# Performance work log

Hardware: AMD Instinct MI355X
Metric: run time of the kernel (lower is better)

Reference implementation:

```python
import jax, jax.numpy as jnp
import numpy as np

B, T, D_MODEL, N_HEADS = 2, 2048, 1024, 16
HEAD_DIM = D_MODEL // N_HEADS
EPS = 1e-6
ROPE_BASE = 10000.0


def _rope_cos_sin(seq_len, dim, offset=0, dtype=jnp.float32):
    half = dim // 2
    inv_freq = 1.0 / (ROPE_BASE ** (jnp.arange(half, dtype=jnp.float32) / half))
    pos = jnp.arange(offset, offset + seq_len, dtype=jnp.float32)
    freqs = pos[:, None] * inv_freq[None, :]              # (T, half)
    emb = jnp.concatenate([freqs, freqs], axis=-1)        # (T, dim)
    return jnp.cos(emb).astype(dtype), jnp.sin(emb).astype(dtype)


def _rotate_half(x):
    x1, x2 = jnp.split(x, 2, axis=-1)
    return jnp.concatenate([-x2, x1], axis=-1)


def setup_inputs() -> dict:
    key = jax.random.key(0)
    k1, k2, k3 = jax.random.split(key, 3)
    x = jax.random.normal(k1, (B, T, D_MODEL), dtype=jnp.float32)
    norm_w = jnp.ones((D_MODEL,), dtype=jnp.float32)
    w_qkv = jax.random.normal(k2, (3 * D_MODEL, D_MODEL), dtype=jnp.float32) * 0.02
    w_out = jax.random.normal(k3, (D_MODEL, D_MODEL), dtype=jnp.float32) * 0.02
    return {"x": x, "norm_w": norm_w, "w_qkv": w_qkv, "w_out": w_out}


def reference(x, norm_w, w_qkv, w_out):
    # RMSNorm (pre-norm)
    h = x * jax.lax.rsqrt(jnp.mean(jnp.square(x), axis=-1, keepdims=True) + EPS) * norm_w
    # Fused QKV projection: (B,T,3*D)
    qkv = jnp.einsum('btd,ed->bte', h, w_qkv).reshape(B, T, 3, N_HEADS, HEAD_DIM)
    q, k, v = qkv[:, :, 0], qkv[:, :, 1], qkv[:, :, 2]   # each (B,T,H,Dh)
    # RoPE on q, k (offset=0)
    cos, sin = _rope_cos_sin(T, HEAD_DIM, dtype=q.dtype)
    cos = cos[None, :, None, :]
    sin = sin[None, :, None, :]
    q = q * cos + _rotate_half(q) * sin
    k = k * cos + _rotate_half(k) * sin
    # Causal scaled dot-product attention
    scale = 1.0 / np.sqrt(HEAD_DIM)
    scores = jnp.einsum('bqhd,bkhd->bhqk', q, k) * scale  # (B,H,T,T)
    causal = jnp.tril(jnp.ones((T, T), dtype=bool))
    scores = jnp.where(causal[None, None], scores, jnp.finfo(scores.dtype).min)
    attn = jax.nn.softmax(scores, axis=-1)
    out = jnp.einsum('bhqk,bkhd->bqhd', attn, v).reshape(B, T, D_MODEL)
    out = jnp.einsum('btd,ed->bte', out, w_out)
    return x + out
```

## Files before the change

### kernel.cpp

```cpp
#include <hip/hip_runtime.h>
#include <math.h>

typedef unsigned short u16;
typedef unsigned int u32;
typedef __attribute__((ext_vector_type(4))) float f32x4;
typedef __attribute__((ext_vector_type(8))) short s16x8;

#define GLL16(g, l) __builtin_amdgcn_global_load_lds( \
    (const __attribute__((address_space(1))) void*)(g), \
    (__attribute__((address_space(3))) void*)(l), 16, 0, 0)

__device__ __forceinline__ u16 f2bf(float f) {
  union { float f; u32 u; } v; v.f = f;
  u32 r = v.u + 0x7FFFu + ((v.u >> 16) & 1u);
  return (u16)(r >> 16);
}
__device__ __forceinline__ float bf2f(u16 h) {
  union { u32 u; float f; } v; v.u = ((u32)h) << 16;
  return v.f;
}
__device__ __forceinline__ u32 pk2bf(float lo, float hi) {
  union { float f; u32 u; } a, b; a.f = lo; b.f = hi;
  return __builtin_amdgcn_perm(b.u + 0x8000u, a.u + 0x8000u, 0x07060302u);
}
__device__ __forceinline__ float fexp2(float x) {
#if __has_builtin(__builtin_amdgcn_exp2f)
  return __builtin_amdgcn_exp2f(x);
#else
  return exp2f(x);
#endif
}

__global__ __launch_bounds__(256) void cast_kernel(const float* __restrict__ src,
                                                   u16* __restrict__ dst, int n4) {
  int i = blockIdx.x * 256 + threadIdx.x;
  if (i >= n4) return;
  float4 v = ((const float4*)src)[i];
  uint2 o;
  o.x = (u32)f2bf(v.x) | ((u32)f2bf(v.y) << 16);
  o.y = (u32)f2bf(v.z) | ((u32)f2bf(v.w) << 16);
  ((uint2*)dst)[i] = o;
}

__global__ __launch_bounds__(256) void rmsnorm_kernel(const float* __restrict__ x,
                                                      const float* __restrict__ wgt,
                                                      u16* __restrict__ h) {
  const int row = blockIdx.x, tid = threadIdx.x;
  const float4 v = *(const float4*)&x[(size_t)row * 1024 + tid * 4];
  float ss = v.x * v.x + v.y * v.y + v.z * v.z + v.w * v.w;
  ss += __shfl_xor(ss, 1);  ss += __shfl_xor(ss, 2);  ss += __shfl_xor(ss, 4);
  ss += __shfl_xor(ss, 8);  ss += __shfl_xor(ss, 16); ss += __shfl_xor(ss, 32);
  __shared__ float red[4];
  if ((tid & 63) == 0) red[tid >> 6] = ss;
  __syncthreads();
  const float tot = red[0] + red[1] + red[2] + red[3];
  const float s = rsqrtf(tot * (1.0f / 1024.0f) + 1e-6f);
  const float4 g = *(const float4*)&wgt[tid * 4];
  uint2 o;
  o.x = (u32)f2bf(v.x * s * g.x) | ((u32)f2bf(v.y * s * g.y) << 16);
  o.y = (u32)f2bf(v.z * s * g.z) | ((u32)f2bf(v.w * s * g.w) << 16);
  *(uint2*)&h[(size_t)row * 1024 + tid * 4] = o;
}

template <int EPI>
__global__ __launch_bounds__(256) void gemm_bt(const u16* __restrict__ A,
                                               const u16* __restrict__ Bt,
                                               u16* __restrict__ Cb,
                                               float* __restrict__ Cf,
                                               const float* __restrict__ resid,
                                               int M, int N, int K) {
  __shared__ __attribute__((aligned(16))) u16 As[128 * 32];
  __shared__ __attribute__((aligned(16))) u16 Bs[128 * 32];
  const int tid = threadIdx.x;
  const int w = tid >> 6, lane = tid & 63;
  const int quad = lane >> 4, l16 = lane & 15;
  const int gm0 = blockIdx.y * 128, gn0 = blockIdx.x * 128;
  const int wm = (w & 1) * 64, wn = (w >> 1) * 64;

  f32x4 acc[4][4] = {};

  for (int k0 = 0; k0 < K; k0 += 32) {
    __syncthreads();
    if (w < 2) {
      #pragma unroll
      for (int i = 0; i < 4; ++i) {
        int sb = (w * 4 + i) * 64;
        int slot = sb + lane;
        int m = slot >> 2, c = (slot & 3) ^ (m & 3);
        GLL16(A + (size_t)(gm0 + m) * K + k0 + c * 8, &As[sb * 8]);
      }
    } else {
      #pragma unroll
      for (int i = 0; i < 4; ++i) {
        int sb = ((w - 2) * 4 + i) * 64;
        int slot = sb + lane;
        int n = slot >> 2, c = (slot & 3) ^ (n & 3);
        GLL16(Bt + (size_t)(gn0 + n) * K + k0 + c * 8, &Bs[sb * 8]);
      }
    }
    __syncthreads();
    s16x8 aF[4], bF[4];
    #pragma unroll
    for (int i = 0; i < 4; ++i) {
      int m = wm + i * 16 + l16;
      aF[i] = *(const s16x8*)&As[(m * 4 + (quad ^ (m & 3))) * 8];
    }
    #pragma unroll
    for (int j = 0; j < 4; ++j) {
      int n = wn + j * 16 + l16;
      bF[j] = *(const s16x8*)&Bs[(n * 4 + (quad ^ (n & 3))) * 8];
    }
    #pragma unroll
    for (int i = 0; i < 4; ++i)
      #pragma unroll
      for (int j = 0; j < 4; ++j)
        acc[i][j] = __builtin_amdgcn_mfma_f32_16x16x32_bf16(aF[i], bF[j], acc[i][j], 0, 0, 0);
  }

  #pragma unroll
  for (int i = 0; i < 4; ++i) {
    int row0 = gm0 + wm + i * 16 + quad * 4;
    #pragma unroll
    for (int j = 0; j < 4; ++j) {
      int col = gn0 + wn + j * 16 + l16;
      #pragma unroll
      for (int r = 0; r < 4; ++r) {
        size_t idx = (size_t)(row0 + r) * N + col;
        if (EPI == 0) Cb[idx] = f2bf(acc[i][j][r]);
        else          Cf[idx] = acc[i][j][r] + resid[idx];
      }
    }
  }
}

__global__ __launch_bounds__(256) void rope_kernel(const u16* __restrict__ qkv,
                                                   u16* __restrict__ Qr,
                                                   u16* __restrict__ Kr,
                                                   u16* __restrict__ Vt) {
  const int tt = blockIdx.x, bh = blockIdx.y;
  const int b = bh >> 4, h = bh & 15;
  const int tid = threadIdx.x;
  const float QSCALE = 0.125f * 1.4426950408889634f;

  #pragma unroll
  for (int ii = 0; ii < 8; ++ii) {
    int idx = ii * 256 + tid;
    int tl = idx >> 5, jj = idx & 31;
    int t = tt * 64 + tl;
    size_t mrow = (size_t)(b * 2048 + t) * 3072 + h * 64;
    float q1 = bf2f(qkv[mrow + jj]),        q2 = bf2f(qkv[mrow + 32 + jj]);
    float k1 = bf2f(qkv[mrow + 1024 + jj]), k2 = bf2f(qkv[mrow + 1024 + 32 + jj]);
    float invf = exp2f(-(float)jj * (13.287712379549449f / 32.0f));
    float ang = (float)t * invf;
    float sn, cs;
    sincosf(ang, &sn, &cs);
    size_t orow = (size_t)(bh * 2048 + t) * 64;
    Qr[orow + jj]      = f2bf((q1 * cs - q2 * sn) * QSCALE);
    Qr[orow + 32 + jj] = f2bf((q2 * cs + q1 * sn) * QSCALE);
    Kr[orow + jj]      = f2bf(k1 * cs - k2 * sn);
    Kr[orow + 32 + jj] = f2bf(k2 * cs + k1 * sn);
  }

  __shared__ __attribute__((aligned(16))) u16 Vl[64][72];
  for (int s = tid; s < 512; s += 256) {
    int r = s >> 3, c8 = (s & 7) * 8;
    *(uint4*)&Vl[r][c8] =
        *(const uint4*)&qkv[(size_t)(b * 2048 + tt * 64 + r) * 3072 + 2048 + h * 64 + c8];
  }
  __syncthreads();
  for (int s = tid; s < 512; s += 256) {
    int d = s >> 3, t8 = (s & 7) * 8;
    u16 tmp[8];
    #pragma unroll
    for (int k = 0; k < 8; ++k) tmp[k] = Vl[t8 + k][d];
    *(uint4*)&Vt[(size_t)(bh * 64 + d) * 2048 + tt * 64 + t8] = *(uint4*)tmp;
  }
}

__global__ __launch_bounds__(256) void attn_kernel(const u16* __restrict__ Qr,
                                                   const u16* __restrict__ Kr,
                                                   const u16* __restrict__ Vt,
                                                   u16* __restrict__ AO) {
  __shared__ __attribute__((aligned(16))) char smem[51200];
  const int tid = threadIdx.x;
  const int w = tid >> 6, lane = tid & 63;
  const int quad = lane >> 4, l16 = lane & 15;
  const int id = blockIdx.x;
  const int bh = id & 31;
  const int qhv = id >> 5;
  const int qblk = (qhv < 8) ? (15 - 2 * qhv) : (2 * qhv - 16);
  const int b = bh >> 4, h = bh & 15;
  const size_t qkb = (size_t)bh * (2048 * 64);
  const size_t vtb = (size_t)bh * (64 * 2048);
  const int q0 = qblk * 128;
  const int q0w = q0 + w * 32;
  const int jmax = 2 * qblk + 1;
  u16* Pw = (u16*)(smem + 32768 + w * 4608);

  s16x8 bQ[2][2];
  #pragma unroll
  for (int s = 0; s < 2; ++s)
    #pragma unroll
    for (int hf = 0; hf < 2; ++hf)
      bQ[s][hf] = *(const s16x8*)&Qr[qkb + (size_t)(q0w + s * 16 + l16) * 64 + hf * 32 + quad * 8];

  f32x4 O[2][4] = {};
  float l_run[2] = {0.0f, 0.0f};

  const int srow = lane >> 3;
  const int scg = (lane & 7) ^ srow;

  auto STAGE = [&](int jn, int nxt) {
    if (w < 2) {
      #pragma unroll
      for (int ii = 0; ii < 4; ++ii) {
        int i = w * 4 + ii;
        GLL16(Kr + qkb + (size_t)(jn * 64 + i * 8 + srow) * 64 + scg * 8,
              smem + nxt * 8192 + i * 1024);
      }
    } else {
      #pragma unroll
      for (int ii = 0; ii < 4; ++ii) {
        int i = (w - 2) * 4 + ii;
        GLL16(Vt + vtb + (size_t)(i * 8 + srow) * 2048 + jn * 64 + scg * 8,
              smem + 16384 + nxt * 8192 + i * 1024);
      }
    }
  };

  STAGE(0, 0);
  __syncthreads();
  int cur = 0;

  for (int j = 0; j <= jmax; ++j) {
    if (j < jmax) STAGE(j + 1, cur ^ 1);

    if (j * 64 <= q0w + 31) {
      const u16* Kb = (const u16*)(smem + cur * 8192);
      const u16* Vb = (const u16*)(smem + 16384 + cur * 8192);
      const bool masked = (j * 64 + 63 > q0w);
      const int rsw = (l16 & 7);

      s16x8 aK[4][2];
      #pragma unroll
      for (int kt = 0; kt < 4; ++kt)
        #pragma unroll
        for (int hf = 0; hf < 2; ++hf)
          aK[kt][hf] = *(const s16x8*)&Kb[(kt * 16 + l16) * 64 + (((hf * 4 + quad) ^ rsw) * 8)];

      f32x4 S[2][4];
      __builtin_amdgcn_s_setprio(1);
      #pragma unroll
      for (int kt = 0; kt < 4; ++kt)
        #pragma unroll
        for (int s = 0; s < 2; ++s) {
          f32x4 z = {};
          z = __builtin_amdgcn_mfma_f32_16x16x32_bf16(aK[kt][0], bQ[s][0], z, 0, 0, 0);
          S[s][kt] = __builtin_amdgcn_mfma_f32_16x16x32_bf16(aK[kt][1], bQ[s][1], z, 0, 0, 0);
        }
      __builtin_amdgcn_s_setprio(0);

      if (masked) {
        #pragma unroll
        for (int s = 0; s < 2; ++s) {
          int q = q0w + s * 16 + l16;
          #pragma unroll
          for (int kt = 0; kt < 4; ++kt) {
            int key0 = j * 64 + kt * 16 + quad * 4;
            #pragma unroll
            for (int r = 0; r < 4; ++r)
              if (key0 + r > q) S[s][kt][r] = -1e30f;
          }
        }
      }

      #pragma unroll
      for (int s = 0; s < 2; ++s) {
        float sum = 0.0f;
        #pragma unroll
        for (int kt = 0; kt < 4; ++kt) {
          #pragma unroll
          for (int r = 0; r < 4; ++r) {
            float e = fexp2(S[s][kt][r]);
            S[s][kt][r] = e;
            sum += e;
          }
        }
        sum += __shfl_xor(sum, 16);
        sum += __shfl_xor(sum, 32);
        l_run[s] += sum;
        #pragma unroll
        for (int kt = 0; kt < 4; ++kt) {
          uint2 pw;
          pw.x = pk2bf(S[s][kt][0], S[s][kt][1]);
          pw.y = pk2bf(S[s][kt][2], S[s][kt][3]);
          *(uint2*)&Pw[s * 1152 + l16 * 72 + kt * 16 + quad * 4] = pw;
        }
      }

      s16x8 bP[2][2];
      #pragma unroll
      for (int s = 0; s < 2; ++s) {
        bP[s][0] = *(const s16x8*)&Pw[s * 1152 + l16 * 72 + quad * 8];
        bP[s][1] = *(const s16x8*)&Pw[s * 1152 + l16 * 72 + 32 + quad * 8];
      }
      s16x8 aV[4][2];
      #pragma unroll
      for (int dt = 0; dt < 4; ++dt)
        #pragma unroll
        for (int hf = 0; hf < 2; ++hf)
          aV[dt][hf] = *(const s16x8*)&Vb[(dt * 16 + l16) * 64 + (((hf * 4 + quad) ^ rsw) * 8)];

      __builtin_amdgcn_s_setprio(1);
      #pragma unroll
      for (int dt = 0; dt < 4; ++dt)
        #pragma unroll
        for (int s = 0; s < 2; ++s) {
          O[s][dt] = __builtin_amdgcn_mfma_f32_16x16x32_bf16(aV[dt][0], bP[s][0], O[s][dt], 0, 0, 0);
          O[s][dt] = __builtin_amdgcn_mfma_f32_16x16x32_bf16(aV[dt][1], bP[s][1], O[s][dt], 0, 0, 0);
        }
      __builtin_amdgcn_s_setprio(0);
    }

    __syncthreads();
    cur ^= 1;
  }

  #pragma unroll
  for (int s = 0; s < 2; ++s) {
    float inv = __builtin_amdgcn_rcpf(l_run[s]);
    int q = q0w + s * 16 + l16;
    #pragma unroll
    for (int dt = 0; dt < 4; ++dt) {
      uint2 ow;
      ow.x = pk2bf(O[s][dt][0] * inv, O[s][dt][1] * inv);
      ow.y = pk2bf(O[s][dt][2] * inv, O[s][dt][3] * inv);
      *(uint2*)&AO[(size_t)(b * 2048 + q) * 1024 + h * 64 + dt * 16 + quad * 4] = ow;
    }
  }
}

extern "C" void kernel_launch(void* const* d_in, const int* in_sizes, int n_in,
                              void* d_out, int out_size, void* d_ws, size_t ws_size,
                              hipStream_t stream) {
  const float* x      = (const float*)d_in[0];
  const float* norm_w = (const float*)d_in[1];
  const float* w_qkv  = (const float*)d_in[2];
  const float* w_out  = (const float*)d_in[3];
  float* out = (float*)d_out;

  u16* ws     = (u16*)d_ws;
  u16* wqkv_b = ws;
  u16* wout_b = wqkv_b + 3145728;
  u16* h_b    = wout_b + 1048576;
  u16* qkv_b  = h_b + 4194304;
  u16* Qr     = qkv_b + 12582912;
  u16* Kr     = Qr + 4194304;
  u16* Vt     = Kr + 4194304;
  u16* AO     = Vt + 4194304;

  cast_kernel<<<3072, 256, 0, stream>>>(w_qkv, wqkv_b, 786432);
  cast_kernel<<<1024, 256, 0, stream>>>(w_out, wout_b, 262144);
  rmsnorm_kernel<<<4096, 256, 0, stream>>>(x, norm_w, h_b);
  gemm_bt<0><<<dim3(24, 32), 256, 0, stream>>>(h_b, wqkv_b, qkv_b, nullptr, nullptr,
                                               4096, 3072, 1024);
  rope_kernel<<<dim3(32, 32), 256, 0, stream>>>(qkv_b, Qr, Kr, Vt);
  attn_kernel<<<512, 256, 0, stream>>>(Qr, Kr, Vt, AO);
  gemm_bt<1><<<dim3(8, 32), 256, 0, stream>>>(AO, wout_b, nullptr, out, x,
                                              4096, 1024, 1024);
}
```

Before: 196.5 us.

## Split attention KV range across two wave groups and pair causal query blocks

The attention kernel now uses 512 threads per block: two groups of four waves each process alternating 64-key tiles for the same 128-query block and merge their partial O and row sums through shared memory at the end. Each block also handles a pair of complementary query blocks (c and 15-c) in sequence, which balances the causal work, and the grid shrinks to 256 blocks. The aim is more parallelism per query block and better load balance. The cost is double the LDS footprint (100KB), an extra reduction pass, and lower block count, which may hurt occupancy.

Result: faster. 190.8 us (-2.9%).

```diff
diff --git a/kernel.cpp b/kernel.cpp
--- a/kernel.cpp
+++ b/kernel.cpp
@@ -177,166 +177,190 @@
   }
 }
 
-__global__ __launch_bounds__(256) void attn_kernel(const u16* __restrict__ Qr,
+__global__ __launch_bounds__(512) void attn_kernel(const u16* __restrict__ Qr,
                                                    const u16* __restrict__ Kr,
                                                    const u16* __restrict__ Vt,
                                                    u16* __restrict__ AO) {
-  __shared__ __attribute__((aligned(16))) char smem[51200];
+  __shared__ __attribute__((aligned(16))) char smem[102400];
   const int tid = threadIdx.x;
   const int w = tid >> 6, lane = tid & 63;
+  const int wq = w & 3, wp = w >> 2;
   const int quad = lane >> 4, l16 = lane & 15;
   const int id = blockIdx.x;
   const int bh = id & 31;
-  const int qhv = id >> 5;
-  const int qblk = (qhv < 8) ? (15 - 2 * qhv) : (2 * qhv - 16);
+  const int c  = id >> 5;
   const int b = bh >> 4, h = bh & 15;
   const size_t qkb = (size_t)bh * (2048 * 64);
   const size_t vtb = (size_t)bh * (64 * 2048);
-  const int q0 = qblk * 128;
-  const int q0w = q0 + w * 32;
-  const int jmax = 2 * qblk + 1;
-  u16* Pw = (u16*)(smem + 32768 + w * 4608);
-
-  s16x8 bQ[2][2];
-  #pragma unroll
-  for (int s = 0; s < 2; ++s)
-    #pragma unroll
-    for (int hf = 0; hf < 2; ++hf)
-      bQ[s][hf] = *(const s16x8*)&Qr[qkb + (size_t)(q0w + s * 16 + l16) * 64 + hf * 32 + quad * 8];
-
-  f32x4 O[2][4] = {};
-  float l_run[2] = {0.0f, 0.0f};
+  u16* Pw = (u16*)(smem + 65536 + w * 4608);
 
   const int srow = lane >> 3;
-  const int scg = (lane & 7) ^ srow;
-
-  auto STAGE = [&](int jn, int nxt) {
-    if (w < 2) {
+  const int scg  = (lane & 7) ^ srow;
+  const int smat = w & 1, stp = (w >> 1) & 1, shalf = (w >> 2) & 1;
+
+  auto STAGE = [&](int j0, int d) {
+    const int jn = j0 + stp;
+    if (smat == 0) {
       #pragma unroll
       for (int ii = 0; ii < 4; ++ii) {
-        int i = w * 4 + ii;
+        int i = shalf * 4 + ii;
         GLL16(Kr + qkb + (size_t)(jn * 64 + i * 8 + srow) * 64 + scg * 8,
-              smem + nxt * 8192 + i * 1024);
+              smem + (stp * 2 + d) * 8192 + i * 1024);
       }
     } else {
       #pragma unroll
       for (int ii = 0; ii < 4; ++ii) {
-        int i = (w - 2) * 4 + ii;
+        int i = shalf * 4 + ii;
         GLL16(Vt + vtb + (size_t)(i * 8 + srow) * 2048 + jn * 64 + scg * 8,
-              smem + 16384 + nxt * 8192 + i * 1024);
+              smem + 32768 + (stp * 2 + d) * 8192 + i * 1024);
       }
     }
   };
 
-  STAGE(0, 0);
-  __syncthreads();
-  int cur = 0;
-
-  for (int j = 0; j <= jmax; ++j) {
-    if (j < jmax) STAGE(j + 1, cur ^ 1);
-
-    if (j * 64 <= q0w + 31) {
-      const u16* Kb = (const u16*)(smem + cur * 8192);
-      const u16* Vb = (const u16*)(smem + 16384 + cur * 8192);
-      const bool masked = (j * 64 + 63 > q0w);
-      const int rsw = (l16 & 7);
-
-      s16x8 aK[4][2];
-      #pragma unroll
-      for (int kt = 0; kt < 4; ++kt)
-        #pragma unroll
-        for (int hf = 0; hf < 2; ++hf)
-          aK[kt][hf] = *(const s16x8*)&Kb[(kt * 16 + l16) * 64 + (((hf * 4 + quad) ^ rsw) * 8)];
-
-      f32x4 S[2][4];
-      __builtin_amdgcn_s_setprio(1);
-      #pragma unroll
-      for (int kt = 0; kt < 4; ++kt)
+  for (int t = 0; t < 2; ++t) {
+    const int qblk = t ? (15 - c) : c;
+    const int q0w = qblk * 128 + wq * 32;
+    const int steps = qblk + 1;
+
+    s16x8 bQ[2][2];
+    #pragma unroll
+    for (int s = 0; s < 2; ++s)
+      #pragma unroll
+      for (int hf = 0; hf < 2; ++hf)
+        bQ[s][hf] = *(const s16x8*)&Qr[qkb + (size_t)(q0w + s * 16 + l16) * 64 + hf * 32 + quad * 8];
+
+    f32x4 O[2][4] = {};
+    float l_run[2] = {0.0f, 0.0f};
+
+    STAGE(0, 0);
+    __syncthreads();
+
+    for (int st = 0; st < steps; ++st) {
+      const int cur = st & 1;
+      if (st + 1 < steps) STAGE(2 * st + 2, cur ^ 1);
+
+      const int j = 2 * st + wp;
+      if (j * 64 <= q0w + 31) {
+        const u16* Kb = (const u16*)(smem + (wp * 2 + cur) * 8192);
+        const u16* Vb = (const u16*)(smem + 32768 + (wp * 2 + cur) * 8192);
+        const bool masked = (j * 64 + 63 > q0w);
+        const int rsw = (l16 & 7);
+
+        s16x8 aK[4][2];
+        #pragma unroll
+        for (int kt = 0; kt < 4; ++kt)
+          #pragma unroll
+          for (int hf = 0; hf < 2; ++hf)
+            aK[kt][hf] = *(const s16x8*)&Kb[(kt * 16 + l16) * 64 + (((hf * 4 + quad) ^ rsw) * 8)];
+
+        f32x4 S[2][4];
+        __builtin_amdgcn_s_setprio(1);
+        #pragma unroll
+        for (int kt = 0; kt < 4; ++kt)
+          #pragma unroll
+          for (int s = 0; s < 2; ++s) {
+            f32x4 z = {};
+            z = __builtin_amdgcn_mfma_f32_16x16x32_bf16(aK[kt][0], bQ[s][0], z, 0, 0, 0);
+            S[s][kt] = __builtin_amdgcn_mfma_f32_16x16x32_bf16(aK[kt][1], bQ[s][1], z, 0, 0, 0);
+          }
+        __builtin_amdgcn_s_setprio(0);
+
+        if (masked) {
+          #pragma unroll
+          for (int s = 0; s < 2; ++s) {
+            int q = q0w + s * 16 + l16;
+            #pragma unroll
+            for (int kt = 0; kt < 4; ++kt) {
+              int key0 = j * 64 + kt * 16 + quad * 4;
+              #pragma unroll
+              for (int r = 0; r < 4; ++r)
+                if (key0 + r > q) S[s][kt][r] = -1e30f;
+            }
+          }
+        }
+
         #pragma unroll
         for (int s = 0; s < 2; ++s) {
-          f32x4 z = {};
-          z = __builtin_amdgcn_mfma_f32_16x16x32_bf16(aK[kt][0], bQ[s][0], z, 0, 0, 0);
-          S[s][kt] = __builtin_amdgcn_mfma_f32_16x16x32_bf16(aK[kt][1], bQ[s][1], z, 0, 0, 0);
+          float sum = 0.0f;
+          #pragma unroll
+          for (int kt = 0; kt < 4; ++kt) {
+            #pragma unroll
+            for (int r = 0; r < 4; ++r) {
+              float e = fexp2(S[s][kt][r]);
+              S[s][kt][r] = e;
+              sum += e;
+            }
+          }
+          sum += __shfl_xor(sum, 16);
+          sum += __shfl_xor(sum, 32);
+          l_run[s] += sum;
+          #pragma unroll
+          for (int kt = 0; kt < 4; ++kt) {
+            uint2 pw;
+            pw.x = pk2bf(S[s][kt][0], S[s][kt][1]);
+            pw.y = pk2bf(S[s][kt][2], S[s][kt][3]);
+            *(uint2*)&Pw[s * 1152 + l16 * 72 + kt * 16 + quad * 4] = pw;
+          }
         }
-      __builtin_amdgcn_s_setprio(0);
-
-      if (masked) {
+
+        s16x8 bP[2][2];
         #pragma unroll
         for (int s = 0; s < 2; ++s) {
-          int q = q0w + s * 16 + l16;
-          #pragma unroll
-          for (int kt = 0; kt < 4; ++kt) {
-            int key0 = j * 64 + kt * 16 + quad * 4;
-            #pragma unroll
-            for (int r = 0; r < 4; ++r)
-              if (key0 + r > q) S[s][kt][r] = -1e30f;
-          }
+          bP[s][0] = *(const s16x8*)&Pw[s * 1152 + l16 * 72 + quad * 8];
+          bP[s][1] = *(const s16x8*)&Pw[s * 1152 + l16 * 72 + 32 + quad * 8];
         }
-      }
-
+        s16x8 aV[4][2];
+        #pragma unroll
+        for (int dt = 0; dt < 4; ++dt)
+          #pragma unroll
+          for (int hf = 0; hf < 2; ++hf)
+            aV[dt][hf] = *(const s16x8*)&Vb[(dt * 16 + l16) * 64 + (((hf * 4 + quad) ^ rsw) * 8)];
+
+        __builtin_amdgcn_s_setprio(1);
+        #pragma unroll
+        for (int dt = 0; dt < 4; ++dt)
+          #pragma unroll
+          for (int s = 0; s < 2; ++s) {
+            O[s][dt] = __builtin_amdgcn_mfma_f32_16x16x32_bf16(aV[dt][0], bP[s][0], O[s][dt], 0, 0, 0);
+            O[s][dt] = __builtin_amdgcn_mfma_f32_16x16x32_bf16(aV[dt][1], bP[s][1], O[s][dt], 0, 0, 0);
+          }
+        __builtin_amdgcn_s_setprio(0);
+      }
+
+      __syncthreads();
+    }
+
+    if (wp == 1) {
+      float* Lsl = (float*)(smem + 65536 + wq * 512);
+      Lsl[lane]      = l_run[0];
+      Lsl[64 + lane] = l_run[1];
+      f32x4* slot = (f32x4*)smem + wq * 512;
+      #pragma unroll
+      for (int s = 0; s < 2; ++s)
+        #pragma unroll
+        for (int dt = 0; dt < 4; ++dt)
+          slot[(s * 4 + dt) * 64 + lane] = O[s][dt];
+    }
+    __syncthreads();
+    if (wp == 0) {
+      const float* Lsl = (const float*)(smem + 65536 + wq * 512);
+      const f32x4* slot = (const f32x4*)smem + wq * 512;
       #pragma unroll
       for (int s = 0; s < 2; ++s) {
-        float sum = 0.0f;
-        #pragma unroll
-        for (int kt = 0; kt < 4; ++kt) {
-          #pragma unroll
-          for (int r = 0; r < 4; ++r) {
-            float e = fexp2(S[s][kt][r]);
-            S[s][kt][r] = e;
-            sum += e;
-          }
+        float l_tot = l_run[s] + Lsl[s * 64 + lane];
+        float inv = __builtin_amdgcn_rcpf(l_tot);
+        int q = q0w + s * 16 + l16;
+        #pragma unroll
+        for (int dt = 0; dt < 4; ++dt) {
+          f32x4 o = O[s][dt] + slot[(s * 4 + dt) * 64 + lane];
+          uint2 ow;
+          ow.x = pk2bf(o[0] * inv, o[1] * inv);
+          ow.y = pk2bf(o[2] * inv, o[3] * inv);
+          *(uint2*)&AO[(size_t)(b * 2048 + q) * 1024 + h * 64 + dt * 16 + quad * 4] = ow;
         }
-        sum += __shfl_xor(sum, 16);
-        sum += __shfl_xor(sum, 32);
-        l_run[s] += sum;
-        #pragma unroll
-        for (int kt = 0; kt < 4; ++kt) {
-          uint2 pw;
-          pw.x = pk2bf(S[s][kt][0], S[s][kt][1]);
-          pw.y = pk2bf(S[s][kt][2], S[s][kt][3]);
-          *(uint2*)&Pw[s * 1152 + l16 * 72 + kt * 16 + quad * 4] = pw;
-        }
-      }
-
-      s16x8 bP[2][2];
-      #pragma unroll
-      for (int s = 0; s < 2; ++s) {
-        bP[s][0] = *(const s16x8*)&Pw[s * 1152 + l16 * 72 + quad * 8];
-        bP[s][1] = *(const s16x8*)&Pw[s * 1152 + l16 * 72 + 32 + quad * 8];
-      }
-      s16x8 aV[4][2];
-      #pragma unroll
-      for (int dt = 0; dt < 4; ++dt)
-        #pragma unroll
-        for (int hf = 0; hf < 2; ++hf)
-          aV[dt][hf] = *(const s16x8*)&Vb[(dt * 16 + l16) * 64 + (((hf * 4 + quad) ^ rsw) * 8)];
-
-      __builtin_amdgcn_s_setprio(1);
-      #pragma unroll
-      for (int dt = 0; dt < 4; ++dt)
-        #pragma unroll
-        for (int s = 0; s < 2; ++s) {
-          O[s][dt] = __builtin_amdgcn_mfma_f32_16x16x32_bf16(aV[dt][0], bP[s][0], O[s][dt], 0, 0, 0);
-          O[s][dt] = __builtin_amdgcn_mfma_f32_16x16x32_bf16(aV[dt][1], bP[s][1], O[s][dt], 0, 0, 0);
-        }
-      __builtin_amdgcn_s_setprio(0);
-    }
-
-    __syncthreads();
-    cur ^= 1;
-  }
-
-  #pragma unroll
-  for (int s = 0; s < 2; ++s) {
-    float inv = __builtin_amdgcn_rcpf(l_run[s]);
-    int q = q0w + s * 16 + l16;
-    #pragma unroll
-    for (int dt = 0; dt < 4; ++dt) {
-      uint2 ow;
-      ow.x = pk2bf(O[s][dt][0] * inv, O[s][dt][1] * inv);
-      ow.y = pk2bf(O[s][dt][2] * inv, O[s][dt][3] * inv);
-      *(uint2*)&AO[(size_t)(b * 2048 + q) * 1024 + h * 64 + dt * 16 + quad * 4] = ow;
-    }
+      }
+    }
+    __syncthreads();
   }
 }
 
@@ -365,7 +389,7 @@
   gemm_bt<0><<<dim3(24, 32), 256, 0, stream>>>(h_b, wqkv_b, qkv_b, nullptr, nullptr,
                                                4096, 3072, 1024);
   rope_kernel<<<dim3(32, 32), 256, 0, stream>>>(qkv_b, Qr, Kr, Vt);
-  attn_kernel<<<512, 256, 0, stream>>>(Qr, Kr, Vt, AO);
+  attn_kernel<<<256, 512, 0, stream>>>(Qr, Kr, Vt, AO);
   gemm_bt<1><<<dim3(8, 32), 256, 0, stream>>>(AO, wout_b, nullptr, out, x,
                                               4096, 1024, 1024);
 }
```
